# Optimization experiments

Measured on AMD Instinct MI355X. Metric: run time of the kernel, lower is better.

## Reference

```python
import jax, jax.numpy as jnp
import numpy as np

NUM_HEADS = 32
NUM_KV_HEADS = 8
HEAD_DIM = 96
ROPE_BASE = 10000.0


def setup_inputs() -> dict:
    key = jax.random.key(0)
    k1, k2, k3 = jax.random.split(key, 3)
    B, S, H = 2, 2048, 3072
    op_size = NUM_HEADS * HEAD_DIM + 2 * NUM_KV_HEADS * HEAD_DIM  # 4608
    hidden_states = jax.random.normal(k1, (B, S, H), dtype=jnp.float32)
    w_qkv = jax.random.normal(k2, (op_size, H), dtype=jnp.float32) * (H ** -0.5)
    w_o = jax.random.normal(k3, (H, H), dtype=jnp.float32) * (H ** -0.5)
    position_ids = jnp.broadcast_to(jnp.arange(S, dtype=jnp.int64), (B, S))
    return {"hidden_states": hidden_states, "position_ids": position_ids,
            "w_qkv": w_qkv, "w_o": w_o}


def _rotate_half(x):
    x1, x2 = jnp.split(x, 2, axis=-1)
    return jnp.concatenate((-x2, x1), axis=-1)


def reference(hidden_states, position_ids, w_qkv, w_o):
    B, S, H = hidden_states.shape
    nh, nkv, hd = NUM_HEADS, NUM_KV_HEADS, HEAD_DIM
    n_rep = nh // nkv

    # fused QKV projection (torch Linear: x @ W^T)
    qkv = jnp.einsum('bsh,oh->bso', hidden_states, w_qkv)
    q_pos = nh * hd
    q = qkv[..., :q_pos].reshape(B, S, nh, hd).transpose(0, 2, 1, 3)
    k = qkv[..., q_pos:q_pos + nkv * hd].reshape(B, S, nkv, hd).transpose(0, 2, 1, 3)
    v = qkv[..., q_pos + nkv * hd:].reshape(B, S, nkv, hd).transpose(0, 2, 1, 3)

    # rotary embedding (Phi3RotaryEmbedding, rope_scaling=None)
    inv_freq = 1.0 / (ROPE_BASE ** (jnp.arange(0, hd, 2, dtype=jnp.float32) / hd))
    freqs = position_ids.astype(jnp.float32)[:, :, None] * inv_freq[None, None, :]  # [B,S,hd/2]
    emb = jnp.concatenate((freqs, freqs), axis=-1)  # [B,S,hd]
    cos = jnp.cos(emb)[:, None, :, :]  # unsqueeze head dim
    sin = jnp.sin(emb)[:, None, :, :]
    q = q * cos + _rotate_half(q) * sin
    k = k * cos + _rotate_half(k) * sin

    # repeat_kv: (B, nkv, S, hd) -> (B, nh, S, hd)
    k = jnp.repeat(k, n_rep, axis=1)
    v = jnp.repeat(v, n_rep, axis=1)

    # causal SDPA
    scale = 1.0 / jnp.sqrt(jnp.float32(hd))
    scores = jnp.einsum('bhqd,bhkd->bhqk', q, k) * scale
    causal = jnp.tril(jnp.ones((S, S), dtype=bool))
    scores = jnp.where(causal[None, None], scores, jnp.finfo(scores.dtype).min)
    probs = jax.nn.softmax(scores, axis=-1)
    attn = jnp.einsum('bhqk,bhkd->bhqd', probs, v)  # [B,nh,S,hd]

    attn = attn.transpose(0, 2, 1, 3).reshape(B, S, nh * hd)
    return jnp.einsum('bsh,oh->bso', attn, w_o)
```

## Files before the change

### kernel.cpp

```cpp
#include <hip/hip_runtime.h>
#include <stdint.h>
#include <math.h>

#define B_   2
#define S_   2048
#define H_   3072
#define NH   32
#define NKV  8
#define HD   96
#define OPSZ 4608
#define MM   (B_*S_)

typedef __attribute__((ext_vector_type(8))) short short8;
typedef __attribute__((ext_vector_type(4))) float floatx4;

__device__ __forceinline__ short f2bf(float f) {
    union { float f; uint32_t u; } v; v.f = f;
    uint32_t r = v.u + 0x7fffu + ((v.u >> 16) & 1u);
    return (short)(r >> 16);
}
__device__ __forceinline__ float bf2f(short s) {
    union { uint32_t u; float f; } v; v.u = ((uint32_t)(uint16_t)s) << 16;
    return v.f;
}
__device__ __forceinline__ uint32_t pk_bf_trunc(float lo, float hi) {
    union { float f; uint32_t u; } a, b; a.f = lo; b.f = hi;
    return (a.u >> 16) | (b.u & 0xFFFF0000u);
}
__device__ __forceinline__ float fast_exp2(float x) {
    float r;
    asm volatile("v_exp_f32 %0, %1" : "=v"(r) : "v"(x));
    return r;
}
__device__ __forceinline__ float dpp_max16(float x) {
    union { float f; int i; } a, t;
    a.f = x;
    t.i = __builtin_amdgcn_update_dpp(0, a.i, 0x128, 0xF, 0xF, false); a.f = fmaxf(a.f, t.f);
    t.i = __builtin_amdgcn_update_dpp(0, a.i, 0x124, 0xF, 0xF, false); a.f = fmaxf(a.f, t.f);
    t.i = __builtin_amdgcn_update_dpp(0, a.i, 0x122, 0xF, 0xF, false); a.f = fmaxf(a.f, t.f);
    t.i = __builtin_amdgcn_update_dpp(0, a.i, 0x121, 0xF, 0xF, false); a.f = fmaxf(a.f, t.f);
    return a.f;
}

__device__ __forceinline__ void async_load16(const void* g, void* l) {
    __builtin_amdgcn_global_load_lds(
        (const __attribute__((address_space(1))) void*)g,
        (__attribute__((address_space(3))) void*)l, 16, 0, 0);
}

#define CN1 (MM * H_ / 4)
#define CN2 (OPSZ * H_ / 4)
#define CN3 (H_ * H_ / 4)
__global__ void cast3_f32_bf16(const float* __restrict__ s1, const float* __restrict__ s2,
                               const float* __restrict__ s3, short* __restrict__ d1,
                               short* __restrict__ d2, short* __restrict__ d3) {
    int gid = blockIdx.x * blockDim.x + threadIdx.x;
    int stride = gridDim.x * blockDim.x;
    for (int i = gid; i < CN1; i += stride) {
        float4 v = ((const float4*)s1)[i];
        short4 o; o.x = f2bf(v.x); o.y = f2bf(v.y); o.z = f2bf(v.z); o.w = f2bf(v.w);
        ((short4*)d1)[i] = o;
    }
    for (int i = gid; i < CN2; i += stride) {
        float4 v = ((const float4*)s2)[i];
        short4 o; o.x = f2bf(v.x); o.y = f2bf(v.y); o.z = f2bf(v.z); o.w = f2bf(v.w);
        ((short4*)d2)[i] = o;
    }
    for (int i = gid; i < CN3; i += stride) {
        float4 v = ((const float4*)s3)[i];
        short4 o; o.x = f2bf(v.x); o.y = f2bf(v.y); o.z = f2bf(v.z); o.w = f2bf(v.w);
        ((short4*)d3)[i] = o;
    }
}

template<int BN, int OUT_BF16>
__global__ __launch_bounds__(512, 2) void gemmN(const short* __restrict__ A, const short* __restrict__ Bm,
                                                float* __restrict__ Cf, short* __restrict__ Cb,
                                                int M, int N, int K) {
    constexpr int NF    = BN / 32;
    constexpr int G     = NF / 3;
    constexpr int BSUB  = BN / 8;
    constexpr int BBY   = BN * 128;
    constexpr int JB    = (BSUB + 7) / 8;
    constexpr int VMN   = (BN == 288) ? 8 : 7;
    __shared__ __align__(16) char smem[65536 + 2 * BBY];
    const int tid = threadIdx.x;
    const int w = tid >> 6, l = tid & 63;
    const int L15 = l & 15, quad = l >> 4;
    const int wr = w & 3, wc = w >> 2;

    const int gm = M >> 8;
    const int nwg = gridDim.x;
    const int id = blockIdx.x;
    const int qq = nwg >> 3, rr = nwg & 7;
    const int xcd = id & 7, sidx = id >> 3;
    const int wgid = (xcd < rr ? xcd * (qq + 1) : rr * (qq + 1) + (xcd - rr) * qq) + sidx;
    const int m0 = (wgid % gm) << 8;
    const int n0 = (wgid / gm) * BN;

    const int cbl = ((l & 3) * 16) ^ (((l >> 5) & 1) << 5);
    uint32_t aofs[4], bofs[JB];
    #pragma unroll
    for (int j = 0; j < 4; j++) {
        const int s = j * 8 + w;
        const int row = ((s >> 1) << 4) + (l >> 2);
        const int colb = ((s & 1) << 6) + cbl;
        aofs[j] = (uint32_t)(m0 + row) * (uint32_t)(K * 2) + colb;
    }
    #pragma unroll
    for (int j = 0; j < JB; j++) {
        const int s = j * 8 + w;
        const int sc = (s < BSUB) ? s : 0;
        const int row = ((sc >> 1) << 4) + (l >> 2);
        const int colb = ((sc & 1) << 6) + cbl;
        bofs[j] = (uint32_t)(n0 + row) * (uint32_t)(K * 2) + colb;
    }
    char* ldsA = (char*)smem;
    char* ldsB = (char*)smem + 65536;

    const int lane_off = L15 * 64 + ((quad * 16) ^ (((L15 >> 3) & 1) << 5));
    const int aoff = (wr * 4) * 2048 + lane_off;
    const int boff = (wc * NF) * 2048 + lane_off;

    floatx4 acc[4][NF];
    #pragma unroll
    for (int i = 0; i < 4; i++)
        #pragma unroll
        for (int j = 0; j < NF; j++)
            acc[i][j] = (floatx4){0.f, 0.f, 0.f, 0.f};

    auto stageA = [&](int kt, int buf) {
        const uint32_t kb = (uint32_t)kt << 7;
        #pragma unroll
        for (int j = 0; j < 4; j++)
            async_load16((const char*)A + (size_t)(aofs[j] + kb),
                         ldsA + buf * 32768 + (j * 8 + w) * 1024);
    };
    auto stageB = [&](int kt, int buf) {
        const uint32_t kb = (uint32_t)kt << 7;
        #pragma unroll
        for (int j = 0; j < JB; j++)
            if (j * 8 + w < BSUB)
                async_load16((const char*)Bm + (size_t)(bofs[j] + kb),
                             ldsB + buf * BBY + (j * 8 + w) * 1024);
    };

    const int nkt = K >> 6;
    stageB(0, 0); stageA(0, 0);
    stageB(1, 1); stageA(1, 1);

    for (int t = 0; t < nkt; t++) {
        const int c = t & 1;
        const char* ab = ldsA + c * 32768 + aoff;
        const char* bb = ldsB + c * BBY + boff;

        if (BN == 288) asm volatile("s_waitcnt vmcnt(8)" ::: "memory");
        else           asm volatile("s_waitcnt vmcnt(7)" ::: "memory");
        __builtin_amdgcn_s_barrier();
        __builtin_amdgcn_sched_barrier(0);

        short8 a[4][2], bg0[G][2], bg1[G][2], bg2[G][2];
        #pragma unroll
        for (int i = 0; i < 4; i++)
            #pragma unroll
            for (int kk = 0; kk < 2; kk++)
                a[i][kk] = *(const short8*)(ab + i * 2048 + kk * 1024);
        #pragma unroll
        for (int g = 0; g < G; g++)
            #pragma unroll
            for (int kk = 0; kk < 2; kk++)
                bg0[g][kk] = *(const short8*)(bb + g * 2048 + kk * 1024);
        #pragma unroll
        for (int g = 0; g < G; g++)
            #pragma unroll
            for (int kk = 0; kk < 2; kk++)
                bg1[g][kk] = *(const short8*)(bb + (G + g) * 2048 + kk * 1024);
        __builtin_amdgcn_s_setprio(1);
        #pragma unroll
        for (int kk = 0; kk < 2; kk++)
            #pragma unroll
            for (int i = 0; i < 4; i++)
                #pragma unroll
                for (int g = 0; g < G; g++)
                    acc[i][g] = __builtin_amdgcn_mfma_f32_16x16x32_bf16(a[i][kk], bg0[g][kk], acc[i][g], 0, 0, 0);
        __builtin_amdgcn_s_setprio(0);
        #pragma unroll
        for (int g = 0; g < G; g++)
            #pragma unroll
            for (int kk = 0; kk < 2; kk++)
                bg2[g][kk] = *(const short8*)(bb + (2 * G + g) * 2048 + kk * 1024);
        __builtin_amdgcn_s_setprio(1);
        #pragma unroll
        for (int kk = 0; kk < 2; kk++)
            #pragma unroll
            for (int i = 0; i < 4; i++)
                #pragma unroll
                for (int g = 0; g < G; g++)
                    acc[i][G + g] = __builtin_amdgcn_mfma_f32_16x16x32_bf16(a[i][kk], bg1[g][kk], acc[i][G + g], 0, 0, 0);
        __builtin_amdgcn_s_setprio(0);
        __builtin_amdgcn_sched_barrier(0);
        __builtin_amdgcn_s_barrier();
        __builtin_amdgcn_sched_barrier(0);
        if (t + 2 < nkt) { stageB(t + 2, c); stageA(t + 2, c); }
        __builtin_amdgcn_s_setprio(1);
        #pragma unroll
        for (int kk = 0; kk < 2; kk++)
            #pragma unroll
            for (int i = 0; i < 4; i++)
                #pragma unroll
                for (int g = 0; g < G; g++)
                    acc[i][2 * G + g] = __builtin_amdgcn_mfma_f32_16x16x32_bf16(a[i][kk], bg2[g][kk], acc[i][2 * G + g], 0, 0, 0);
        __builtin_amdgcn_s_setprio(0);
    }
    asm volatile("s_waitcnt vmcnt(0)" ::: "memory");

    #pragma unroll
    for (int i = 0; i < 4; i++)
        #pragma unroll
        for (int j = 0; j < NF; j++)
            #pragma unroll
            for (int r = 0; r < 4; r++) {
                const int row = m0 + wr * 64 + i * 16 + quad * 4 + r;
                const int col = n0 + wc * (BN / 2) + j * 16 + L15;
                const float v = acc[i][j][r];
                if (OUT_BF16) Cb[(size_t)row * N + col] = f2bf(v);
                else          Cf[(size_t)row * N + col] = v;
            }
}

__global__ void rope_reorder(const short* __restrict__ qkv, const int* __restrict__ pos_ids,
                             short* __restrict__ Q, short* __restrict__ Kc) {
    const int total = B_ * S_ * (NH + NKV) * HD;
    int idx = blockIdx.x * blockDim.x + threadIdx.x;
    int stride = gridDim.x * blockDim.x;
    for (; idx < total; idx += stride) {
        int d = idx % HD;
        int row = idx / HD;
        int h_all = row % (NH + NKV);
        int sb = row / (NH + NKV);
        int s = sb % S_;
        int b = sb / S_;
        int base = (b * S_ + s) * OPSZ;
        int off = (h_all < NH) ? (h_all * HD + d) : (H_ + (h_all - NH) * HD + d);
        float x = bf2f(qkv[base + off]);
        int delta = (d < 48) ? 48 : -48;
        float x2 = bf2f(qkv[base + off + delta]);
        int fi = d % 48;
        float inv = exp2f((float)fi * -0.2768273412f);
        float theta = (float)pos_ids[b * S_ + s] * inv;
        float sn, cs;
        __sincosf(theta, &sn, &cs);
        float rot = (d < 48) ? -x2 : x2;
        float outv = x * cs + rot * sn;
        if (h_all < NH) {
            outv *= 0.14724438747f;
            Q[((size_t)(b * NH + h_all) * S_ + s) * HD + d] = f2bf(outv);
        } else {
            int kvh = h_all - NH;
            size_t kaddr = ((size_t)(b * NKV + kvh) * S_ + s) * 128
                         + (((d >> 3) + s) & 15) * 8 + (d & 7);
            Kc[kaddr] = f2bf(outv);
        }
    }
}

__global__ __launch_bounds__(256) void v_transpose(const short* __restrict__ qkv, short* __restrict__ Vt) {
    __shared__ short tile[64 * 104];
    int blk = blockIdx.x;
    int st  = blk & 31;
    int kvh = (blk >> 5) & 7;
    int b   = blk >> 8;
    int s0  = st * 64;
    int tid = threadIdx.x;
    #pragma unroll
    for (int i = 0; i < 3; i++) {
        int c = tid + i * 256;
        int row = c / 12, col8 = c % 12;
        *(short8*)&tile[row * 104 + col8 * 8] =
            *(const short8*)(qkv + (size_t)(b * S_ + s0 + row) * OPSZ + 3840 + kvh * HD + col8 * 8);
    }
    __syncthreads();
    #pragma unroll
    for (int i = 0; i < 3; i++) {
        int c = tid + i * 256;
        int d = c >> 3, col8 = c & 7;
        int chunk0 = (col8 - d) & 7;
        short8 v;
        #pragma unroll
        for (int j = 0; j < 8; j++) {
            int col0 = chunk0 * 8 + j;
            int n = ((col0 >> 5) << 1) | (col0 & 1);
            int t = (col0 & 31) >> 1;
            v[j] = tile[(n * 16 + t) * 104 + d];
        }
        *(short8*)(Vt + ((size_t)(b * NKV + kvh) * HD + d) * S_ + s0 + col8 * 8) = v;
    }
}

__global__ __launch_bounds__(256) void flash_attn(const short* __restrict__ Q, const short* __restrict__ Kc,
                                                  const short* __restrict__ Vt, short* __restrict__ attn) {
    __shared__ short kl[2][64 * 128];
    __shared__ short vl[2][112 * 64];
    __shared__ short pl[4][32 * 72];
    const int x = blockIdx.x, h = blockIdx.y, b = blockIdx.z;
    const int kvh = h >> 2;
    const int tid = threadIdx.x, wave = tid >> 6, lane = tid & 63;
    const int L15 = lane & 15, quad = lane >> 4;

    #pragma unroll
    for (int i = 0; i < 2; i++) {
        uint32_t* p = (uint32_t*)&vl[i][96 * 64];
        #pragma unroll
        for (int k = 0; k < 2; k++) {
            int idx = tid + k * 256;
            p[idx] = (idx < 32) ? 0x3F803F80u : 0u;
        }
    }

    const short* kbase = Kc + (size_t)(b * NKV + kvh) * S_ * 128;
    const short* vbase = Vt + (size_t)(b * NKV + kvh) * HD * S_;
    const int klane   = lane * 8;
    const int vrow_lo = lane >> 3;
    const int vcol    = (lane & 7) * 8;

    int rotK[3], rotV[2];
    #pragma unroll
    for (int kk = 0; kk < 3; kk++) rotK[kk] = ((kk * 4 + quad + L15) & 15) * 8;
    #pragma unroll
    for (int kk = 0; kk < 2; kk++) rotV[kk] = ((kk * 4 + quad + L15) & 7) * 8;

    auto stage = [&](int kv0, int buf) {
        const short* ksrc = kbase + (size_t)kv0 * 128;
        #pragma unroll
        for (int i = 0; i < 4; i++) {
            int ck = wave * 4 + i;
            async_load16(ksrc + ck * 512 + klane, &kl[buf][ck * 512]);
        }
        #pragma unroll
        for (int i = 0; i < 3; i++) {
            int ck = wave * 3 + i;
            async_load16(vbase + (size_t)(ck * 8 + vrow_lo) * S_ + kv0 + vcol, &vl[buf][ck * 512]);
        }
    };

    #pragma unroll
    for (int pp = 0; pp < 2; pp++) {
        const int qt = pp ? x : (15 - x);
        const int q0 = qt * 128;
        const int jmax = 2 * qt + 2;

        short8 qf[2][3];
        #pragma unroll
        for (int mm = 0; mm < 2; mm++) {
            const short* qrow = Q + ((size_t)(b * NH + h) * S_ + q0 + wave * 32 + mm * 16 + L15) * HD;
            #pragma unroll
            for (int kk = 0; kk < 3; kk++) qf[mm][kk] = *(const short8*)(qrow + kk * 32 + quad * 8);
        }
        floatx4 o[2][7];
        float m_r[2][4];
        #pragma unroll
        for (int mm = 0; mm < 2; mm++) {
            #pragma unroll
            for (int nn = 0; nn < 7; nn++) o[mm][nn] = (floatx4){0.f, 0.f, 0.f, 0.f};
            #pragma unroll
            for (int r = 0; r < 4; r++) m_r[mm][r] = -3.0e38f;
        }

        __syncthreads();
        stage(0, 0);

        for (int j = 0; j < jmax; j++) {
            const int c = j & 1;
            const int kv0 = j * 64;
            __syncthreads();
            if (j + 1 < jmax) stage(kv0 + 64, 1 - c);

            const short* klp = kl[c];
            const short* vlp = vl[c];

            floatx4 sacc[2][4];
            #pragma unroll
            for (int mm = 0; mm < 2; mm++)
                #pragma unroll
                for (int n = 0; n < 4; n++) sacc[mm][n] = (floatx4){0.f, 0.f, 0.f, 0.f};
            #pragma unroll
            for (int n = 0; n < 4; n++)
                #pragma unroll
                for (int kk = 0; kk < 3; kk++) {
                    short8 kf = *(const short8*)&klp[(n * 16 + L15) * 128 + rotK[kk]];
                    sacc[0][n] = __builtin_amdgcn_mfma_f32_16x16x32_bf16(qf[0][kk], kf, sacc[0][n], 0, 0, 0);
                    sacc[1][n] = __builtin_amdgcn_mfma_f32_16x16x32_bf16(qf[1][kk], kf, sacc[1][n], 0, 0, 0);
                }

            #pragma unroll
            for (int mm = 0; mm < 2; mm++) {
                const int tbase = q0 + wave * 32 + mm * 16;
                if (kv0 + 63 > tbase) {
                    int qr_base = tbase + quad * 4;
                    #pragma unroll
                    for (int n = 0; n < 4; n++) {
                        int kv = kv0 + n * 16 + L15;
                        #pragma unroll
                        for (int r = 0; r < 4; r++)
                            if (kv > qr_base + r) sacc[mm][n][r] = -3.0e38f;
                    }
                }
                float alpha[4];
                #pragma unroll
                for (int r = 0; r < 4; r++) {
                    float mx = fmaxf(fmaxf(sacc[mm][0][r], sacc[mm][1][r]),
                                     fmaxf(sacc[mm][2][r], sacc[mm][3][r]));
                    mx = dpp_max16(mx);
                    float mn = fmaxf(m_r[mm][r], mx);
                    alpha[r] = fast_exp2(m_r[mm][r] - mn);
                    m_r[mm][r] = mn;
                }
                #pragma unroll
                for (int n = 0; n < 4; n++)
                    #pragma unroll
                    for (int r = 0; r < 4; r++)
                        sacc[mm][n][r] = fast_exp2(sacc[mm][n][r] - m_r[mm][r]);
                #pragma unroll
                for (int r = 0; r < 4; r++) {
                    int prow = mm * 16 + quad * 4 + r;
                    *(uint32_t*)&pl[wave][prow * 72 + 2 * L15]      = pk_bf_trunc(sacc[mm][0][r], sacc[mm][1][r]);
                    *(uint32_t*)&pl[wave][prow * 72 + 32 + 2 * L15] = pk_bf_trunc(sacc[mm][2][r], sacc[mm][3][r]);
                }
                #pragma unroll
                for (int nn = 0; nn < 7; nn++)
                    #pragma unroll
                    for (int r = 0; r < 4; r++) o[mm][nn][r] *= alpha[r];
            }

            #pragma unroll
            for (int kk = 0; kk < 2; kk++) {
                short8 af0 = *(const short8*)&pl[wave][L15 * 72 + kk * 32 + quad * 8];
                short8 af1 = *(const short8*)&pl[wave][(16 + L15) * 72 + kk * 32 + quad * 8];
                #pragma unroll
                for (int nn = 0; nn < 7; nn++) {
                    short8 vf = *(const short8*)&vlp[(nn * 16 + L15) * 64 + rotV[kk]];
                    o[0][nn] = __builtin_amdgcn_mfma_f32_16x16x32_bf16(af0, vf, o[0][nn], 0, 0, 0);
                    o[1][nn] = __builtin_amdgcn_mfma_f32_16x16x32_bf16(af1, vf, o[1][nn], 0, 0, 0);
                }
            }
        }

        #pragma unroll
        for (int mm = 0; mm < 2; mm++) {
            float inv_l[4];
            #pragma unroll
            for (int r = 0; r < 4; r++) {
                float l = __shfl(o[mm][6][r], lane & 48);
                inv_l[r] = 1.0f / l;
            }
            #pragma unroll
            for (int nn = 0; nn < 6; nn++)
                #pragma unroll
                for (int r = 0; r < 4; r++) {
                    float v = o[mm][nn][r] * inv_l[r];
                    int row = q0 + wave * 32 + mm * 16 + quad * 4 + r;
                    attn[((size_t)(b * S_) + row) * H_ + h * HD + nn * 16 + L15] = f2bf(v);
                }
        }
    }
}

extern "C" void kernel_launch(void* const* d_in, const int* in_sizes, int n_in,
                              void* d_out, int out_size, void* d_ws, size_t ws_size,
                              hipStream_t stream) {
    const float* hid  = (const float*)d_in[0];
    const int*   pos  = (const int*)d_in[1];
    const float* wqkv = (const float*)d_in[2];
    const float* wo   = (const float*)d_in[3];
    float* out = (float*)d_out;
    char* ws = (char*)d_ws;

    short* hid_b  = (short*)(ws + 0L);
    short* wqkv_b = (short*)(ws + 25165824L);
    short* wo_b   = (short*)(ws + 53477376L);
    short* qkv_b  = (short*)(ws + 72351744L);
    short* q_b    = (short*)(ws + 110100480L);
    short* k_b    = (short*)(ws + 135266304L);
    short* vt_b   = (short*)(ws + 143654912L);
    short* attn_b = (short*)(ws + 0L);

    cast3_f32_bf16<<<4096, 256, 0, stream>>>(hid, wqkv, wo, hid_b, wqkv_b, wo_b);

    gemmN<288, 1><<<256, 512, 0, stream>>>(hid_b, wqkv_b, nullptr, qkv_b, MM, OPSZ, H_);

    rope_reorder<<<8192, 256, 0, stream>>>(qkv_b, pos, q_b, k_b);
    v_transpose<<<512, 256, 0, stream>>>(qkv_b, vt_b);

    flash_attn<<<dim3(8, NH, B_), 256, 0, stream>>>(q_b, k_b, vt_b, attn_b);

    gemmN<192, 0><<<256, 512, 0, stream>>>(attn_b, wo_b, out, nullptr, MM, H_, H_);
}
```

Before: 474.8 us.

## Add lazy softmax rescaling, MFMA priority, hardware bf16 packing, and precomputed RoPE table

In flash attention, the running-max update and output rescale now run only when some row's max grows by more than a threshold, checked with a wave ballot. Otherwise exponentials use the stale max, which avoids most rescale multiplies and exps. MFMA blocks are wrapped in s_setprio, P is packed with v_cvt_pk_bf16_f32 (rounding) instead of truncation, and the exp asm is no longer volatile. RoPE cos/sin are precomputed into a table by a new small kernel, so they are no longer recomputed per element. The table reuses the start of the workspace that the hidden-state copy and later the attention output occupy, which is safe only if ordering holds.

```diff
diff --git a/kernel.cpp b/kernel.cpp
--- a/kernel.cpp
+++ b/kernel.cpp
@@ -23,13 +23,14 @@
     union { uint32_t u; float f; } v; v.u = ((uint32_t)(uint16_t)s) << 16;
     return v.f;
 }
-__device__ __forceinline__ uint32_t pk_bf_trunc(float lo, float hi) {
-    union { float f; uint32_t u; } a, b; a.f = lo; b.f = hi;
-    return (a.u >> 16) | (b.u & 0xFFFF0000u);
+__device__ __forceinline__ uint32_t cvt_pk_bf16(float lo, float hi) {
+    uint32_t r;
+    asm("v_cvt_pk_bf16_f32 %0, %1, %2" : "=v"(r) : "v"(lo), "v"(hi));
+    return r;
 }
 __device__ __forceinline__ float fast_exp2(float x) {
     float r;
-    asm volatile("v_exp_f32 %0, %1" : "=v"(r) : "v"(x));
+    asm("v_exp_f32 %0, %1" : "=v"(r) : "v"(x));
     return r;
 }
 __device__ __forceinline__ float dpp_max16(float x) {
@@ -82,7 +83,6 @@
     constexpr int BSUB  = BN / 8;
     constexpr int BBY   = BN * 128;
     constexpr int JB    = (BSUB + 7) / 8;
-    constexpr int VMN   = (BN == 288) ? 8 : 7;
     __shared__ __align__(16) char smem[65536 + 2 * BBY];
     const int tid = threadIdx.x;
     const int w = tid >> 6, l = tid & 63;
@@ -228,7 +228,19 @@
             }
 }
 
-__global__ void rope_reorder(const short* __restrict__ qkv, const int* __restrict__ pos_ids,
+#define TABN (B_ * S_ * 48)
+__global__ void rope_tab(const int* __restrict__ pos_ids, float2* __restrict__ tab) {
+    int i = blockIdx.x * blockDim.x + threadIdx.x;
+    if (i >= TABN) return;
+    int fi = i % 48, sb = i / 48;
+    float inv = exp2f((float)fi * -0.2768273412f);
+    float theta = (float)pos_ids[sb] * inv;
+    float sn, cs;
+    __sincosf(theta, &sn, &cs);
+    tab[i] = make_float2(cs, sn);
+}
+
+__global__ void rope_reorder(const short* __restrict__ qkv, const float2* __restrict__ tab,
                              short* __restrict__ Q, short* __restrict__ Kc) {
     const int total = B_ * S_ * (NH + NKV) * HD;
     int idx = blockIdx.x * blockDim.x + threadIdx.x;
@@ -240,18 +252,15 @@
         int sb = row / (NH + NKV);
         int s = sb % S_;
         int b = sb / S_;
-        int base = (b * S_ + s) * OPSZ;
+        int base = sb * OPSZ;
         int off = (h_all < NH) ? (h_all * HD + d) : (H_ + (h_all - NH) * HD + d);
         float x = bf2f(qkv[base + off]);
         int delta = (d < 48) ? 48 : -48;
         float x2 = bf2f(qkv[base + off + delta]);
         int fi = d % 48;
-        float inv = exp2f((float)fi * -0.2768273412f);
-        float theta = (float)pos_ids[b * S_ + s] * inv;
-        float sn, cs;
-        __sincosf(theta, &sn, &cs);
+        float2 t = tab[sb * 48 + fi];
         float rot = (d < 48) ? -x2 : x2;
-        float outv = x * cs + rot * sn;
+        float outv = x * t.x + rot * t.y;
         if (h_all < NH) {
             outv *= 0.14724438747f;
             Q[((size_t)(b * NH + h_all) * S_ + s) * HD + d] = f2bf(outv);
@@ -383,6 +392,7 @@
             for (int mm = 0; mm < 2; mm++)
                 #pragma unroll
                 for (int n = 0; n < 4; n++) sacc[mm][n] = (floatx4){0.f, 0.f, 0.f, 0.f};
+            __builtin_amdgcn_s_setprio(1);
             #pragma unroll
             for (int n = 0; n < 4; n++)
                 #pragma unroll
@@ -391,6 +401,7 @@
                     sacc[0][n] = __builtin_amdgcn_mfma_f32_16x16x32_bf16(qf[0][kk], kf, sacc[0][n], 0, 0, 0);
                     sacc[1][n] = __builtin_amdgcn_mfma_f32_16x16x32_bf16(qf[1][kk], kf, sacc[1][n], 0, 0, 0);
                 }
+            __builtin_amdgcn_s_setprio(0);
 
             #pragma unroll
             for (int mm = 0; mm < 2; mm++) {
@@ -405,15 +416,24 @@
                             if (kv > qr_base + r) sacc[mm][n][r] = -3.0e38f;
                     }
                 }
-                float alpha[4];
+                float mx[4];
                 #pragma unroll
                 for (int r = 0; r < 4; r++) {
-                    float mx = fmaxf(fmaxf(sacc[mm][0][r], sacc[mm][1][r]),
+                    float m4 = fmaxf(fmaxf(sacc[mm][0][r], sacc[mm][1][r]),
                                      fmaxf(sacc[mm][2][r], sacc[mm][3][r]));
-                    mx = dpp_max16(mx);
-                    float mn = fmaxf(m_r[mm][r], mx);
-                    alpha[r] = fast_exp2(m_r[mm][r] - mn);
-                    m_r[mm][r] = mn;
+                    mx[r] = dpp_max16(m4);
+                }
+                float dm = fmaxf(fmaxf(mx[0] - m_r[mm][0], mx[1] - m_r[mm][1]),
+                                 fmaxf(mx[2] - m_r[mm][2], mx[3] - m_r[mm][3]));
+                if (__builtin_amdgcn_ballot_w64(dm > 8.0f)) {
+                    #pragma unroll
+                    for (int r = 0; r < 4; r++) {
+                        float mn = fmaxf(m_r[mm][r], mx[r]);
+                        float alpha = fast_exp2(m_r[mm][r] - mn);
+                        m_r[mm][r] = mn;
+                        #pragma unroll
+                        for (int nn = 0; nn < 7; nn++) o[mm][nn][r] *= alpha;
+                    }
                 }
                 #pragma unroll
                 for (int n = 0; n < 4; n++)
@@ -423,15 +443,12 @@
                 #pragma unroll
                 for (int r = 0; r < 4; r++) {
                     int prow = mm * 16 + quad * 4 + r;
-                    *(uint32_t*)&pl[wave][prow * 72 + 2 * L15]      = pk_bf_trunc(sacc[mm][0][r], sacc[mm][1][r]);
-                    *(uint32_t*)&pl[wave][prow * 72 + 32 + 2 * L15] = pk_bf_trunc(sacc[mm][2][r], sacc[mm][3][r]);
-                }
-                #pragma unroll
-                for (int nn = 0; nn < 7; nn++)
-                    #pragma unroll
-                    for (int r = 0; r < 4; r++) o[mm][nn][r] *= alpha[r];
+                    *(uint32_t*)&pl[wave][prow * 72 + 2 * L15]      = cvt_pk_bf16(sacc[mm][0][r], sacc[mm][1][r]);
+                    *(uint32_t*)&pl[wave][prow * 72 + 32 + 2 * L15] = cvt_pk_bf16(sacc[mm][2][r], sacc[mm][3][r]);
+                }
             }
 
+            __builtin_amdgcn_s_setprio(1);
             #pragma unroll
             for (int kk = 0; kk < 2; kk++) {
                 short8 af0 = *(const short8*)&pl[wave][L15 * 72 + kk * 32 + quad * 8];
@@ -443,6 +460,7 @@
                     o[1][nn] = __builtin_amdgcn_mfma_f32_16x16x32_bf16(af1, vf, o[1][nn], 0, 0, 0);
                 }
             }
+            __builtin_amdgcn_s_setprio(0);
         }
 
         #pragma unroll
@@ -482,13 +500,15 @@
     short* q_b    = (short*)(ws + 110100480L);
     short* k_b    = (short*)(ws + 135266304L);
     short* vt_b   = (short*)(ws + 143654912L);
+    float2* tab   = (float2*)(ws + 0L);
     short* attn_b = (short*)(ws + 0L);
 
     cast3_f32_bf16<<<4096, 256, 0, stream>>>(hid, wqkv, wo, hid_b, wqkv_b, wo_b);
 
     gemmN<288, 1><<<256, 512, 0, stream>>>(hid_b, wqkv_b, nullptr, qkv_b, MM, OPSZ, H_);
 
-    rope_reorder<<<8192, 256, 0, stream>>>(qkv_b, pos, q_b, k_b);
+    rope_tab<<<(TABN + 255) / 256, 256, 0, stream>>>((const int*)d_in[1], tab);
+    rope_reorder<<<8192, 256, 0, stream>>>(qkv_b, tab, q_b, k_b);
     v_transpose<<<512, 256, 0, stream>>>(qkv_b, vt_b);
 
     flash_attn<<<dim3(8, NH, B_), 256, 0, stream>>>(q_b, k_b, vt_b, attn_b);
```

Measured after the change: 524.5 us. 1.1x slower.
